# Performance work log

Hardware: AMD Instinct MI355X
Metric: run time of the kernel (lower is better)

## Reference

```python
import jax, jax.numpy as jnp
import numpy as np

KEEP_P = 0.75  # 1 - dropout_p, dropout_p = 0.25

def setup_inputs() -> dict:
    key = jax.random.key(0)
    k1, k2, k3, k4 = jax.random.split(key, 4)
    B, Sq, Skv, D, Dv = 8, 2048, 2048, 128, 128
    x1 = jax.random.normal(k1, (B, Sq, D), dtype=jnp.float32)
    x2 = jax.random.normal(k2, (B, Skv, D), dtype=jnp.float32)
    x3 = jax.random.normal(k3, (B, Skv, Dv), dtype=jnp.float32)
    # torch Dropout(p): mask = bernoulli(keep_p) / keep_p
    keep = jax.random.bernoulli(k4, KEEP_P, (B, Sq, Skv))
    dropout_mask = keep.astype(jnp.float32) / KEEP_P
    return {"x1": x1, "x2": x2, "x3": x3, "dropout_mask": dropout_mask}

def reference(x1, x2, x3, dropout_mask):
    # scores: [B, Sq, Skv] = x1 @ x2^T (no scale: scale_factor is None)
    scores = jnp.einsum("bqd,bkd->bqk", x1, x2)
    probs = jax.nn.softmax(scores, axis=-1)
    probs = probs * dropout_mask  # dropout with fixed mask
    out = jnp.einsum("bqk,bkv->bqv", probs, x3)  # [B, Sq, Dv]
    return out
```

## Files before the change

### kernel.cpp

```cpp
#include <hip/hip_runtime.h>
#include <stdint.h>

#define SQ 2048
#define SKV 2048
#define DD 128
#define NB 8
#define M0 40.0f
#define LOG2E 1.44269504088896340736f

typedef float    f4v __attribute__((ext_vector_type(4)));
typedef __bf16   bf8 __attribute__((ext_vector_type(8)));
typedef _Float16 h8  __attribute__((ext_vector_type(8)));

__device__ __forceinline__ void async16(const void* g, void* l) {
    __builtin_amdgcn_global_load_lds(
        (const __attribute__((address_space(1))) void*)g,
        (__attribute__((address_space(3))) void*)l, 16, 0, 0);
}

__global__ void cast_f16_swz(const float* __restrict__ src,
                             _Float16* __restrict__ dst) {
    int tid = blockIdx.x * 256 + threadIdx.x;
    int d8 = tid & 15;
    int kv = (tid >> 4) & (SKV - 1);
    int b  = tid >> 15;
    const float* p = src + ((size_t)b * SKV + kv) * DD + d8 * 8;
    f4v a0 = *(const f4v*)p;
    f4v a1 = *(const f4v*)(p + 4);
    h8 h;
#pragma unroll
    for (int c = 0; c < 4; c++) {
        h[c]     = (_Float16)a0[c];
        h[c + 4] = (_Float16)a1[c];
    }
    int s = d8 >> 2, g = d8 & 3, kb32 = kv >> 5, row = kv & 31;
    *(h8*)(dst + (size_t)(b * 64 + kb32) * 4096 + (size_t)((s * 32 + row) * 4 + g) * 8) = h;
}

__global__ void transpose_v_swz(const float* __restrict__ v, __bf16* __restrict__ vtf) {
    __shared__ __bf16 tile[32][33];
    int kb32 = blockIdx.x, dv0 = blockIdx.y * 32, b = blockIdx.z;
    int tx = threadIdx.x, ty = threadIdx.y;
    const float* src = v + ((size_t)b * SKV + kb32 * 32 + ty) * DD + dv0 + tx;
#pragma unroll
    for (int i = 0; i < 32; i += 8)
        tile[ty + i][tx] = (__bf16)src[(size_t)i * DD];
    __syncthreads();
    int pcol = (tx < 16) ? ((tx >> 2) << 3) + (tx & 3)
                         : (((tx - 16) >> 2) << 3) + 4 + (tx & 3);
    __bf16* dst = vtf + (size_t)(b * 64 + kb32) * 4096 + pcol;
#pragma unroll
    for (int i = 0; i < 32; i += 8)
        dst[(size_t)(dv0 + ty + i) * 32] = tile[tx][ty + i];
}

__global__ __launch_bounds__(256, 2) void attn_kernel(
    const float* __restrict__ Qf, const _Float16* __restrict__ Kh,
    const __bf16* __restrict__ Vt, const float* __restrict__ mask,
    float* __restrict__ O_part, float* __restrict__ l_part,
    int nsp, int kv_len) {
    __shared__ __align__(16) char smem[2][16384];
    const int lin = blockIdx.x;
    const int per_xcd = (NB * nsp) >> 3;
    const int xcd = lin & 7;
    const int idx = lin >> 3;
    const int slice = xcd * per_xcd + (idx >> 4);
    const int qblk = idx & 15;
    const int b = slice / nsp, sid = slice % nsp;
    const int tid = threadIdx.x;
    const int w = tid >> 6, lane = tid & 63;
    const int g = lane >> 4, n = lane & 15;
    const int qb = qblk * 128 + w * 32;
    const int kv0 = sid * kv_len;
    const int kb32_0 = kv0 >> 5;
    const int niter = kv_len >> 5;

    const _Float16* Kt0 = Kh + (size_t)(b * 64 + kb32_0) * 4096;
    const __bf16*   Vt0 = Vt + (size_t)(b * 64 + kb32_0) * 4096;
    auto stage = [&](int buf, int it) {
#pragma unroll
        for (int jj = 0; jj < 4; jj++) {
            int j = w * 4 + jj;
            if (j < 8)
                async16(Kt0 + (size_t)it * 4096 + j * 512 + lane * 8,
                        (void*)&smem[buf][j * 1024]);
            else
                async16(Vt0 + (size_t)it * 4096 + (j - 8) * 512 + lane * 8,
                        (void*)&smem[buf][8192 + (j - 8) * 1024]);
        }
    };
    stage(0, 0);

    h8 qf[2][4];
#pragma unroll
    for (int u = 0; u < 2; u++) {
        const float* Qrow = Qf + ((size_t)b * SQ + qb + u * 16 + n) * DD + g * 8;
#pragma unroll
        for (int s = 0; s < 4; s++) {
            f4v v0 = *(const f4v*)(Qrow + s * 32);
            f4v v1 = *(const f4v*)(Qrow + s * 32 + 4);
#pragma unroll
            for (int c = 0; c < 4; c++) {
                qf[u][s][c]     = (_Float16)v0[c];
                qf[u][s][c + 4] = (_Float16)v1[c];
            }
        }
    }

    const float* mrow0 = mask + ((size_t)b * SQ + qb + n) * SKV + kv0;
    const float* mrow1 = mrow0 + (size_t)16 * SKV;
    f4v c00 = *(const f4v*)(mrow0 + g * 4);
    f4v c01 = *(const f4v*)(mrow0 + 16 + g * 4);
    f4v c10 = *(const f4v*)(mrow1 + g * 4);
    f4v c11 = *(const f4v*)(mrow1 + 16 + g * 4);

    const f4v zero = {0.f, 0.f, 0.f, 0.f};
    f4v o0[8], o1[8];
#pragma unroll
    for (int t = 0; t < 8; t++) { o0[t] = zero; o1[t] = zero; }
    float l0 = 0.f, l1 = 0.f;

    for (int it = 0; it < niter; it++) {
        __syncthreads();

        if (it + 1 < niter) stage((it + 1) & 1, it + 1);
        const int itn = (it + 1 < niter) ? it + 1 : it;
        f4v n00 = *(const f4v*)(mrow0 + itn * 32 + g * 4);
        f4v n01 = *(const f4v*)(mrow0 + itn * 32 + 16 + g * 4);
        f4v n10 = *(const f4v*)(mrow1 + itn * 32 + g * 4);
        f4v n11 = *(const f4v*)(mrow1 + itn * 32 + 16 + g * 4);

        const _Float16* Lk = (const _Float16*)smem[it & 1];
        const __bf16*   Lv = (const __bf16*)(smem[it & 1] + 8192);

        f4v s00 = zero, s01 = zero, s10 = zero, s11 = zero;
#pragma unroll
        for (int s = 0; s < 4; s++) {
            h8 a0 = *(const h8*)(Lk + (size_t)((s * 32 + n) * 4 + g) * 8);
            h8 a1 = *(const h8*)(Lk + (size_t)((s * 32 + n + 16) * 4 + g) * 8);
            s00 = __builtin_amdgcn_mfma_f32_16x16x32_f16(a0, qf[0][s], s00, 0, 0, 0);
            s01 = __builtin_amdgcn_mfma_f32_16x16x32_f16(a1, qf[0][s], s01, 0, 0, 0);
            s10 = __builtin_amdgcn_mfma_f32_16x16x32_f16(a0, qf[1][s], s10, 0, 0, 0);
            s11 = __builtin_amdgcn_mfma_f32_16x16x32_f16(a1, qf[1][s], s11, 0, 0, 0);
        }

        bf8 pf0, pf1;
#pragma unroll
        for (int r = 0; r < 4; r++) {
            float e00 = exp2f(s00[r] * LOG2E - M0 * LOG2E);
            float e01 = exp2f(s01[r] * LOG2E - M0 * LOG2E);
            float e10 = exp2f(s10[r] * LOG2E - M0 * LOG2E);
            float e11 = exp2f(s11[r] * LOG2E - M0 * LOG2E);
            l0 += e00 + e01;
            l1 += e10 + e11;
            pf0[r]     = (__bf16)(e00 * c00[r]);
            pf0[r + 4] = (__bf16)(e01 * c01[r]);
            pf1[r]     = (__bf16)(e10 * c10[r]);
            pf1[r + 4] = (__bf16)(e11 * c11[r]);
        }

#pragma unroll
        for (int t = 0; t < 8; t++) {
            bf8 vf = *(const bf8*)(Lv + (size_t)((t * 16 + n) * 4 + g) * 8);
            o0[t] = __builtin_amdgcn_mfma_f32_16x16x32_bf16(pf0, vf, o0[t], 0, 0, 0);
            o1[t] = __builtin_amdgcn_mfma_f32_16x16x32_bf16(pf1, vf, o1[t], 0, 0, 0);
        }
        c00 = n00; c01 = n01; c10 = n10; c11 = n11;
    }

    l0 += __shfl_xor(l0, 16); l0 += __shfl_xor(l0, 32);
    l1 += __shfl_xor(l1, 16); l1 += __shfl_xor(l1, 32);
    const int qt = qblk * 8 + w * 2;
    const int tile0 = (b * 128 + qt) * nsp + sid;
    const int tile1 = (b * 128 + qt + 1) * nsp + sid;
    float* op0 = O_part + (size_t)tile0 * 2048;
    float* op1 = O_part + (size_t)tile1 * 2048;
#pragma unroll
    for (int t = 0; t < 8; t++)
#pragma unroll
        for (int r = 0; r < 4; r++) {
            op0[(g * 4 + r) * 128 + t * 16 + n] = o0[t][r];
            op1[(g * 4 + r) * 128 + t * 16 + n] = o1[t][r];
        }
    if (g == 0) {
        l_part[(size_t)tile0 * 16 + n] = l0;
        l_part[(size_t)tile1 * 16 + n] = l1;
    }
}

__global__ __launch_bounds__(256) void combine_kernel(
    const float* __restrict__ O_part, const float* __restrict__ l_part,
    float* __restrict__ out, int nsp) {
    const int qt = blockIdx.x;
    const int b  = blockIdx.y;
    const int tbase = (b * 128 + qt) * nsp;
    const int q  = threadIdx.x >> 4;
    const int d8 = threadIdx.x & 15;
    f4v a0 = {0.f, 0.f, 0.f, 0.f}, a1 = {0.f, 0.f, 0.f, 0.f};
    float L = 0.f;
    for (int s = 0; s < nsp; s++) {
        const float* op = O_part + (size_t)(tbase + s) * 2048 + q * 128 + d8 * 8;
        a0 += *(const f4v*)op;
        a1 += *(const f4v*)(op + 4);
        L  += l_part[(size_t)(tbase + s) * 16 + q];
    }
    float scale = 1.0f / L;
    float* o = out + ((size_t)b * SQ + qt * 16 + q) * DD + d8 * 8;
    *(f4v*)o       = a0 * scale;
    *(f4v*)(o + 4) = a1 * scale;
}

extern "C" void kernel_launch(void* const* d_in, const int* in_sizes, int n_in,
                              void* d_out, int out_size, void* d_ws, size_t ws_size,
                              hipStream_t stream) {
    const float* x1   = (const float*)d_in[0];
    const float* x2   = (const float*)d_in[1];
    const float* x3   = (const float*)d_in[2];
    const float* mask = (const float*)d_in[3];
    float* out = (float*)d_out;

    const size_t kelems = (size_t)NB * SKV * DD;
    _Float16* Kh  = (_Float16*)d_ws;
    __bf16*   VTf = (__bf16*)(Kh + kelems);
    float*    O_part = (float*)(VTf + kelems);

    size_t base = 2 * kelems * 2;
    size_t per  = (size_t)NB * 128 * (2048 + 16) * sizeof(float);
    int nsp = 4;
    while (nsp > 1 && base + (size_t)nsp * per > ws_size) nsp >>= 1;
    float* l_part = O_part + (size_t)NB * 128 * nsp * 2048;

    hipLaunchKernelGGL(cast_f16_swz, dim3(NB * SKV * 16 / 256), dim3(256), 0, stream,
                       x2, Kh);
    hipLaunchKernelGGL(transpose_v_swz, dim3(SKV / 32, DD / 32, NB), dim3(32, 8), 0,
                       stream, x3, VTf);
    hipLaunchKernelGGL(attn_kernel, dim3(16 * NB * nsp), dim3(256), 0, stream,
                       x1, Kh, VTf, mask, O_part, l_part, nsp, SKV / nsp);
    hipLaunchKernelGGL(combine_kernel, dim3(128, NB), dim3(256), 0, stream,
                       O_part, l_part, out, nsp);
}
```

Before: 233.6 us.

## Merge preprocessing kernels, re-swizzle K/V LDS layout, raise occupancy and split count

Fuses the K cast and V transpose into one preprocess launch, and changes the swizzled layout of K and V so each lane's LDS fragment reads are laid out with the 16 rows contiguous per group, presumably to reduce bank conflicts. It raises launch bounds from 2 to 4 blocks per CU and doubles the KV split count to 8, giving more parallelism at the cost of more partial outputs for the combine pass and more register pressure. It also precomputes the max-offset constant in log2 units.

```diff
diff --git a/kernel.cpp b/kernel.cpp
--- a/kernel.cpp
+++ b/kernel.cpp
@@ -5,8 +5,8 @@
 #define SKV 2048
 #define DD 128
 #define NB 8
-#define M0 40.0f
 #define LOG2E 1.44269504088896340736f
+#define M0L 57.70780163555852f
 
 typedef float    f4v __attribute__((ext_vector_type(4)));
 typedef __bf16   bf8 __attribute__((ext_vector_type(8)));
@@ -18,43 +18,49 @@
         (__attribute__((address_space(3))) void*)l, 16, 0, 0);
 }
 
-__global__ void cast_f16_swz(const float* __restrict__ src,
-                             _Float16* __restrict__ dst) {
-    int tid = blockIdx.x * 256 + threadIdx.x;
-    int d8 = tid & 15;
-    int kv = (tid >> 4) & (SKV - 1);
-    int b  = tid >> 15;
-    const float* p = src + ((size_t)b * SKV + kv) * DD + d8 * 8;
-    f4v a0 = *(const f4v*)p;
-    f4v a1 = *(const f4v*)(p + 4);
-    h8 h;
-#pragma unroll
-    for (int c = 0; c < 4; c++) {
-        h[c]     = (_Float16)a0[c];
-        h[c + 4] = (_Float16)a1[c];
-    }
-    int s = d8 >> 2, g = d8 & 3, kb32 = kv >> 5, row = kv & 31;
-    *(h8*)(dst + (size_t)(b * 64 + kb32) * 4096 + (size_t)((s * 32 + row) * 4 + g) * 8) = h;
-}
-
-__global__ void transpose_v_swz(const float* __restrict__ v, __bf16* __restrict__ vtf) {
+__global__ void preprocess(const float* __restrict__ x2, _Float16* __restrict__ Kh,
+                           const float* __restrict__ x3, __bf16* __restrict__ VTf) {
     __shared__ __bf16 tile[32][33];
-    int kb32 = blockIdx.x, dv0 = blockIdx.y * 32, b = blockIdx.z;
-    int tx = threadIdx.x, ty = threadIdx.y;
-    const float* src = v + ((size_t)b * SKV + kb32 * 32 + ty) * DD + dv0 + tx;
-#pragma unroll
-    for (int i = 0; i < 32; i += 8)
-        tile[ty + i][tx] = (__bf16)src[(size_t)i * DD];
-    __syncthreads();
-    int pcol = (tx < 16) ? ((tx >> 2) << 3) + (tx & 3)
-                         : (((tx - 16) >> 2) << 3) + 4 + (tx & 3);
-    __bf16* dst = vtf + (size_t)(b * 64 + kb32) * 4096 + pcol;
-#pragma unroll
-    for (int i = 0; i < 32; i += 8)
-        dst[(size_t)(dv0 + ty + i) * 32] = tile[tx][ty + i];
-}
-
-__global__ __launch_bounds__(256, 2) void attn_kernel(
+    const int bid = blockIdx.x;
+    if (bid < 1024) {
+        int tid = bid * 256 + threadIdx.x;
+        int d8 = tid & 15;
+        int kv = (tid >> 4) & (SKV - 1);
+        int b  = tid >> 15;
+        const float* p = x2 + ((size_t)b * SKV + kv) * DD + d8 * 8;
+        f4v a0 = *(const f4v*)p;
+        f4v a1 = *(const f4v*)(p + 4);
+        h8 h;
+#pragma unroll
+        for (int c = 0; c < 4; c++) {
+            h[c]     = (_Float16)a0[c];
+            h[c + 4] = (_Float16)a1[c];
+        }
+        int s = d8 >> 2, g = d8 & 3, kb32 = kv >> 5, row = kv & 31;
+        int h8idx = s * 128 + ((row >> 4) << 6) + g * 16 + (row & 15);
+        *(h8*)(Kh + (size_t)(b * 64 + kb32) * 4096 + (size_t)h8idx * 8) = h;
+    } else {
+        int t = bid - 1024;
+        int kb32 = t & 63, dv0 = ((t >> 6) & 3) * 32, b = t >> 8;
+        int tx = threadIdx.x & 31, ty = threadIdx.x >> 5;
+        const float* src = x3 + ((size_t)b * SKV + kb32 * 32 + ty) * DD + dv0 + tx;
+#pragma unroll
+        for (int i = 0; i < 32; i += 8)
+            tile[ty + i][tx] = (__bf16)src[(size_t)i * DD];
+        __syncthreads();
+        int pcol = (tx < 16) ? ((tx >> 2) << 3) + (tx & 3)
+                             : (((tx - 16) >> 2) << 3) + 4 + (tx & 3);
+        __bf16* base = VTf + (size_t)(b * 64 + kb32) * 4096
+                     + ((pcol >> 3) << 7) + (pcol & 7);
+#pragma unroll
+        for (int i = 0; i < 32; i += 8) {
+            int dv = dv0 + ty + i;
+            base[((dv >> 4) << 9) + ((dv & 15) << 3)] = tile[tx][ty + i];
+        }
+    }
+}
+
+__global__ __launch_bounds__(256, 4) void attn_kernel(
     const float* __restrict__ Qf, const _Float16* __restrict__ Kh,
     const __bf16* __restrict__ Vt, const float* __restrict__ mask,
     float* __restrict__ O_part, float* __restrict__ l_part,
@@ -122,7 +128,6 @@
 
     for (int it = 0; it < niter; it++) {
         __syncthreads();
-
         if (it + 1 < niter) stage((it + 1) & 1, it + 1);
         const int itn = (it + 1 < niter) ? it + 1 : it;
         f4v n00 = *(const f4v*)(mrow0 + itn * 32 + g * 4);
@@ -136,8 +141,8 @@
         f4v s00 = zero, s01 = zero, s10 = zero, s11 = zero;
 #pragma unroll
         for (int s = 0; s < 4; s++) {
-            h8 a0 = *(const h8*)(Lk + (size_t)((s * 32 + n) * 4 + g) * 8);
-            h8 a1 = *(const h8*)(Lk + (size_t)((s * 32 + n + 16) * 4 + g) * 8);
+            h8 a0 = *(const h8*)(Lk + (size_t)(s * 128 + g * 16 + n) * 8);
+            h8 a1 = *(const h8*)(Lk + (size_t)(s * 128 + 64 + g * 16 + n) * 8);
             s00 = __builtin_amdgcn_mfma_f32_16x16x32_f16(a0, qf[0][s], s00, 0, 0, 0);
             s01 = __builtin_amdgcn_mfma_f32_16x16x32_f16(a1, qf[0][s], s01, 0, 0, 0);
             s10 = __builtin_amdgcn_mfma_f32_16x16x32_f16(a0, qf[1][s], s10, 0, 0, 0);
@@ -147,10 +152,10 @@
         bf8 pf0, pf1;
 #pragma unroll
         for (int r = 0; r < 4; r++) {
-            float e00 = exp2f(s00[r] * LOG2E - M0 * LOG2E);
-            float e01 = exp2f(s01[r] * LOG2E - M0 * LOG2E);
-            float e10 = exp2f(s10[r] * LOG2E - M0 * LOG2E);
-            float e11 = exp2f(s11[r] * LOG2E - M0 * LOG2E);
+            float e00 = exp2f(s00[r] * LOG2E - M0L);
+            float e01 = exp2f(s01[r] * LOG2E - M0L);
+            float e10 = exp2f(s10[r] * LOG2E - M0L);
+            float e11 = exp2f(s11[r] * LOG2E - M0L);
             l0 += e00 + e01;
             l1 += e10 + e11;
             pf0[r]     = (__bf16)(e00 * c00[r]);
@@ -161,7 +166,7 @@
 
 #pragma unroll
         for (int t = 0; t < 8; t++) {
-            bf8 vf = *(const bf8*)(Lv + (size_t)((t * 16 + n) * 4 + g) * 8);
+            bf8 vf = *(const bf8*)(Lv + (size_t)(t * 64 + g * 16 + n) * 8);
             o0[t] = __builtin_amdgcn_mfma_f32_16x16x32_bf16(pf0, vf, o0[t], 0, 0, 0);
             o1[t] = __builtin_amdgcn_mfma_f32_16x16x32_bf16(pf1, vf, o1[t], 0, 0, 0);
         }
@@ -226,14 +231,12 @@
 
     size_t base = 2 * kelems * 2;
     size_t per  = (size_t)NB * 128 * (2048 + 16) * sizeof(float);
-    int nsp = 4;
+    int nsp = 8;
     while (nsp > 1 && base + (size_t)nsp * per > ws_size) nsp >>= 1;
     float* l_part = O_part + (size_t)NB * 128 * nsp * 2048;
 
-    hipLaunchKernelGGL(cast_f16_swz, dim3(NB * SKV * 16 / 256), dim3(256), 0, stream,
-                       x2, Kh);
-    hipLaunchKernelGGL(transpose_v_swz, dim3(SKV / 32, DD / 32, NB), dim3(32, 8), 0,
-                       stream, x3, VTf);
+    hipLaunchKernelGGL(preprocess, dim3(3072), dim3(256), 0, stream,
+                       x2, Kh, x3, VTf);
     hipLaunchKernelGGL(attn_kernel, dim3(16 * NB * nsp), dim3(256), 0, stream,
                        x1, Kh, VTf, mask, O_part, l_part, nsp, SKV / nsp);
     hipLaunchKernelGGL(combine_kernel, dim3(128, NB), dim3(256), 0, stream,
```

Result: slower. 309.7 us (+32.6%).
